# Kernel tuning notes

Hardware: AMD Instinct MI355X
Metric: run time of the kernel (lower is better)

## Reference

```python
import jax, jax.numpy as jnp
import numpy as np

BN_EPS = 1e-5
NN_EPS = 1e-8

def _bn_relu(h, gamma, beta):
    # training-mode BatchNorm1d over (B, L) per channel, biased variance
    mean = jnp.mean(h, axis=(0, 2), keepdims=True)
    var = jnp.mean((h - mean) ** 2, axis=(0, 2), keepdims=True)
    hn = (h - mean) * jax.lax.rsqrt(var + BN_EPS)
    return jax.nn.relu(hn * gamma[None, :, None] + beta[None, :, None])

def setup_inputs() -> dict:
    key = jax.random.key(0)
    ks = jax.random.split(key, 8)
    B, N, M, Cin, Cout = 2, 2048, 8192, 512, 256
    return {
        "x1": jax.random.normal(ks[0], (B, N, Cin), jnp.float32),
        "p1": jax.random.uniform(ks[1], (B, N, 3), jnp.float32),
        "x2": jax.random.normal(ks[2], (B, M, Cout), jnp.float32),
        "p2": jax.random.uniform(ks[3], (B, M, 3), jnp.float32),
        "W_up": jax.random.normal(ks[4], (Cout, Cin), jnp.float32) * (1.0 / np.sqrt(Cin)),
        "gamma_up": jnp.ones((Cout,), jnp.float32),
        "beta_up": jnp.zeros((Cout,), jnp.float32),
        "W_lat": jax.random.normal(ks[5], (Cout, Cout), jnp.float32) * (1.0 / np.sqrt(Cout)),
        "gamma_lat": jnp.ones((Cout,), jnp.float32),
        "beta_lat": jnp.zeros((Cout,), jnp.float32),
    }

def reference(x1, p1, x2, p2, W_up, gamma_up, beta_up, W_lat, gamma_lat, beta_lat):
    B, M, _ = p2.shape
    # up_mlp: 1x1 conv (bias=False) + BN + ReLU -> (B, Cout, N)
    h1 = _bn_relu(jnp.einsum('bnc,oc->bon', x1, W_up), gamma_up, beta_up)
    # three_nn: squared distances from each p2 query to all p1 points
    d2 = (jnp.sum(p2 ** 2, -1)[:, :, None] + jnp.sum(p1 ** 2, -1)[:, None, :]
          - 2.0 * jnp.einsum('bmd,bnd->bmn', p2, p1))  # (B, M, N)
    neg_d, idx = jax.lax.top_k(-d2, 3)                 # 3 smallest squared dists
    dist = -neg_d                                      # (B, M, 3)
    dist_recip = 1.0 / (dist + NN_EPS)
    weight = dist_recip / jnp.sum(dist_recip, axis=2, keepdims=True)  # (B, M, 3)
    # three_interpolate: weighted gather of h1 along point axis
    C = h1.shape[1]
    g = jnp.take_along_axis(h1, idx.reshape(B, 1, M * 3), axis=2).reshape(B, C, M, 3)
    interp = jnp.einsum('bcmk,bmk->bcm', g, weight)    # (B, Cout, M)
    # lateral_mlp on x2
    h2 = _bn_relu(jnp.einsum('bmc,oc->bom', x2, W_lat), gamma_lat, beta_lat)
    y = interp + h2                                    # (B, Cout, M)
    return jnp.transpose(y, (0, 2, 1)), p2             # (B, M, Cout), (B, M, 3)
```

## Files before the change

kernel.cpp:

```cpp
#include <hip/hip_runtime.h>

#define BATCH 2
#define NPTS  2048
#define MPTS  8192
#define CIN1  512
#define CIN2  256
#define COUT  256
#define ROWS1 (BATCH*NPTS)
#define ROWS2 (BATCH*MPTS)
#define BN_EPS 1e-5f
#define NN_EPS 1e-8f

#define NCHUNK 16
#define CHUNK  (NPTS / NCHUNK)

typedef __attribute__((ext_vector_type(8))) short  bf16x8;
typedef __attribute__((ext_vector_type(4))) float  f32x4;

__device__ __forceinline__ unsigned short bf16_rne(float x) {
    unsigned u = __float_as_uint(x);
    u += 0x7FFFu + ((u >> 16) & 1u);
    return (unsigned short)(u >> 16);
}
__device__ __forceinline__ float bf16_f32(unsigned short h) {
    return __uint_as_float(((unsigned)h) << 16);
}
__device__ __forceinline__ void split2(float x, unsigned short& h, unsigned short& l) {
    h = bf16_rne(x);
    l = bf16_rne(x - bf16_f32(h));
}

template<int K, int KSPLIT, bool FUSE_STATS>
__global__ __launch_bounds__(256)
void gemm_mfma64(const float* __restrict__ A, const float* __restrict__ W,
                 float* __restrict__ C, float* __restrict__ stats) {
    constexpr int BK = 32;
    constexpr int LDK = 40;
    constexpr int KCH = K / KSPLIT;
    __shared__ unsigned short Ah[64][LDK], Al[64][LDK];
    __shared__ unsigned short Bh[64][LDK], Bl[64][LDK];
    __shared__ float red[64][8];

    const int tid = threadIdx.x;
    const int m0 = blockIdx.y * 64;
    const int o0 = blockIdx.x * 64;
    const int kbase = blockIdx.z * KCH;
    const int lane = tid & 63, wid = tid >> 6;
    const int wy = wid >> 1, wx = wid & 1;
    const int lr = lane & 15, lg = lane >> 4;
    const int srow = tid >> 3;
    const int squad = (tid & 7) * 4;

    f32x4 acc[2][2];
    #pragma unroll
    for (int i = 0; i < 2; ++i)
        #pragma unroll
        for (int j = 0; j < 2; ++j)
            acc[i][j] = (f32x4){0.f, 0.f, 0.f, 0.f};

    const float* Abase = A + (size_t)m0 * K + kbase + squad;
    const float* Wbase = W + (size_t)o0 * K + kbase + squad;

    for (int k0 = 0; k0 < KCH; k0 += BK) {
        __syncthreads();
        #pragma unroll
        for (int rr = 0; rr < 2; ++rr) {
            const int r = srow + rr * 32;
            float4 va = *(const float4*)(Abase + (size_t)r * K + k0);
            float4 vb = *(const float4*)(Wbase + (size_t)r * K + k0);
            ushort4 h, l;
            split2(va.x, h.x, l.x); split2(va.y, h.y, l.y);
            split2(va.z, h.z, l.z); split2(va.w, h.w, l.w);
            *(ushort4*)&Ah[r][squad] = h;
            *(ushort4*)&Al[r][squad] = l;
            split2(vb.x, h.x, l.x); split2(vb.y, h.y, l.y);
            split2(vb.z, h.z, l.z); split2(vb.w, h.w, l.w);
            *(ushort4*)&Bh[r][squad] = h;
            *(ushort4*)&Bl[r][squad] = l;
        }
        __syncthreads();

        bf16x8 fah[2], fal[2], fbh[2], fbl[2];
        #pragma unroll
        for (int i = 0; i < 2; ++i) {
            const int row = wy * 32 + i * 16 + lr;
            fah[i] = *(const bf16x8*)&Ah[row][lg * 8];
            fal[i] = *(const bf16x8*)&Al[row][lg * 8];
        }
        #pragma unroll
        for (int j = 0; j < 2; ++j) {
            const int row = wx * 32 + j * 16 + lr;
            fbh[j] = *(const bf16x8*)&Bh[row][lg * 8];
            fbl[j] = *(const bf16x8*)&Bl[row][lg * 8];
        }
        #pragma unroll
        for (int i = 0; i < 2; ++i)
            #pragma unroll
            for (int j = 0; j < 2; ++j) {
                acc[i][j] = __builtin_amdgcn_mfma_f32_16x16x32_bf16(fah[i], fbh[j], acc[i][j], 0, 0, 0);
                acc[i][j] = __builtin_amdgcn_mfma_f32_16x16x32_bf16(fal[i], fbh[j], acc[i][j], 0, 0, 0);
                acc[i][j] = __builtin_amdgcn_mfma_f32_16x16x32_bf16(fah[i], fbl[j], acc[i][j], 0, 0, 0);
            }
    }

    #pragma unroll
    for (int i = 0; i < 2; ++i)
        #pragma unroll
        for (int j = 0; j < 2; ++j) {
            const int col = o0 + wx * 32 + j * 16 + lr;
            const int rbase = m0 + wy * 32 + i * 16 + lg * 4;
            #pragma unroll
            for (int r = 0; r < 4; ++r) {
                if (KSPLIT > 1)
                    atomicAdd(&C[(size_t)(rbase + r) * COUT + col], acc[i][j][r]);
                else
                    C[(size_t)(rbase + r) * COUT + col] = acc[i][j][r];
            }
        }

    if constexpr (FUSE_STATS) {
        #pragma unroll
        for (int j = 0; j < 2; ++j) {
            float s = 0.f;
            #pragma unroll
            for (int i = 0; i < 2; ++i)
                #pragma unroll
                for (int r = 0; r < 4; ++r)
                    s += acc[i][j][r];
            red[wx * 32 + j * 16 + lr][wy * 4 + lg] = s;
        }
        __syncthreads();
        if (tid < 64) {
            float s = 0.f;
            #pragma unroll
            for (int k = 0; k < 8; ++k) s += red[tid][k];
            atomicAdd(&stats[o0 + tid], s);
        }
        __syncthreads();
        #pragma unroll
        for (int j = 0; j < 2; ++j) {
            float q = 0.f;
            #pragma unroll
            for (int i = 0; i < 2; ++i)
                #pragma unroll
                for (int r = 0; r < 4; ++r)
                    q = fmaf(acc[i][j][r], acc[i][j][r], q);
            red[wx * 32 + j * 16 + lr][wy * 4 + lg] = q;
        }
        __syncthreads();
        if (tid < 64) {
            float q = 0.f;
            #pragma unroll
            for (int k = 0; k < 8; ++k) q += red[tid][k];
            atomicAdd(&stats[COUT + o0 + tid], q);
        }
    }
}

__global__ __launch_bounds__(256)
void colsum256(const float* __restrict__ X, int rowsPerBlock,
               float* __restrict__ out) {
    const int c = threadIdx.x;
    const int r0 = blockIdx.x * rowsPerBlock;
    float s = 0.f, q = 0.f;
    for (int r = 0; r < rowsPerBlock; ++r) {
        float v = X[(size_t)(r0 + r) * COUT + c];
        s += v;
        q = fmaf(v, v, q);
    }
    atomicAdd(&out[c], s);
    atomicAdd(&out[COUT + c], q);
}

__global__ __launch_bounds__(256)
void three_nn_part(const float* __restrict__ p1, const float* __restrict__ p2,
                   float2* __restrict__ part) {
    __shared__ float4 pts[CHUNK];
    const int b = blockIdx.z;
    const int c = blockIdx.y;
    const int t = threadIdx.x;
    const int n0 = c * CHUNK;
    if (t < CHUNK) {
        const float* P1 = p1 + ((size_t)b * NPTS + n0) * 3;
        float x = P1[t * 3 + 0], y = P1[t * 3 + 1], z = P1[t * 3 + 2];
        pts[t] = make_float4(x, y, z, x * x + y * y + z * z);
    }
    __syncthreads();
    const int m = blockIdx.x * 256 + t;
    const float* q = p2 + ((size_t)b * MPTS + m) * 3;
    const float qx = q[0], qy = q[1], qz = q[2];
    const float s2 = qx * qx + qy * qy + qz * qz;
    float d0 = 1e30f, d1 = 1e30f, d2 = 1e30f;
    int   i0 = 0,     i1 = 0,     i2 = 0;
    #pragma unroll 4
    for (int n = 0; n < CHUNK; ++n) {
        float4 p = pts[n];
        float dot = p.x * qx + p.y * qy + p.z * qz;
        float d = s2 + p.w - 2.0f * dot;
        if (d < d2) {
            if (d < d1) {
                d2 = d1; i2 = i1;
                if (d < d0) { d1 = d0; i1 = i0; d0 = d; i0 = n0 + n; }
                else        { d1 = d;  i1 = n0 + n; }
            } else { d2 = d; i2 = n0 + n; }
        }
    }
    float2* o = part + ((size_t)(b * MPTS + m) * NCHUNK + c) * 3;
    o[0] = make_float2(d0, __int_as_float(i0));
    o[1] = make_float2(d1, __int_as_float(i1));
    o[2] = make_float2(d2, __int_as_float(i2));
}

__global__ __launch_bounds__(256)
void three_nn_merge(const float2* __restrict__ part,
                    int* __restrict__ idx, float* __restrict__ wgt) {
    const int row = blockIdx.x * 256 + threadIdx.x;
    const float4* pp = (const float4*)(part + (size_t)row * NCHUNK * 3);
    float d0 = 1e30f, d1 = 1e30f, d2 = 1e30f;
    int   i0 = 0,     i1 = 0,     i2 = 0;
    #pragma unroll
    for (int j = 0; j < NCHUNK * 3 / 2; ++j) {
        float4 v = pp[j];
        #pragma unroll
        for (int h = 0; h < 2; ++h) {
            float d = h ? v.z : v.x;
            int   i = __float_as_int(h ? v.w : v.y);
            if (d < d2) {
                if (d < d1) {
                    d2 = d1; i2 = i1;
                    if (d < d0) { d1 = d0; i1 = i0; d0 = d; i0 = i; }
                    else        { d1 = d;  i1 = i; }
                } else { d2 = d; i2 = i; }
            }
        }
    }
    const float r0 = 1.0f / (d0 + NN_EPS);
    const float r1 = 1.0f / (d1 + NN_EPS);
    const float r2 = 1.0f / (d2 + NN_EPS);
    const float rs = r0 + r1 + r2;
    const size_t o = (size_t)row * 3;
    idx[o + 0] = i0; idx[o + 1] = i1; idx[o + 2] = i2;
    wgt[o + 0] = r0 / rs; wgt[o + 1] = r1 / rs; wgt[o + 2] = r2 / rs;
}

__global__ __launch_bounds__(256)
void final_combine(const float* __restrict__ h1, const float* __restrict__ stats,
                   const float* __restrict__ g1, const float* __restrict__ b1,
                   const float* __restrict__ g2, const float* __restrict__ b2,
                   const int* __restrict__ idx, const float* __restrict__ wgt,
                   float* __restrict__ out) {
    const int t = threadIdx.x;
    const int row = blockIdx.x * 4 + (t >> 6);
    const int c = (t & 63) * 4;
    const int b = row >> 13;

    const float4 sum1 = *(const float4*)&stats[c];
    const float4 sq1  = *(const float4*)&stats[COUT + c];
    const float4 sum2 = *(const float4*)&stats[512 + c];
    const float4 sq2  = *(const float4*)&stats[768 + c];
    const float4 gg1  = *(const float4*)&g1[c];
    const float4 bb1  = *(const float4*)&b1[c];
    const float4 gg2  = *(const float4*)&g2[c];
    const float4 bb2  = *(const float4*)&b2[c];

    const float inv1 = 1.0f / (float)ROWS1, inv2 = 1.0f / (float)ROWS2;
    float4 sc1, sh1, sc2, sh2;
    {
        float m, v;
        m = sum1.x*inv1; v = fmaf(-m,m,sq1.x*inv1); sc1.x = gg1.x/sqrtf(v+BN_EPS); sh1.x = fmaf(-m,sc1.x,bb1.x);
        m = sum1.y*inv1; v = fmaf(-m,m,sq1.y*inv1); sc1.y = gg1.y/sqrtf(v+BN_EPS); sh1.y = fmaf(-m,sc1.y,bb1.y);
        m = sum1.z*inv1; v = fmaf(-m,m,sq1.z*inv1); sc1.z = gg1.z/sqrtf(v+BN_EPS); sh1.z = fmaf(-m,sc1.z,bb1.z);
        m = sum1.w*inv1; v = fmaf(-m,m,sq1.w*inv1); sc1.w = gg1.w/sqrtf(v+BN_EPS); sh1.w = fmaf(-m,sc1.w,bb1.w);
        m = sum2.x*inv2; v = fmaf(-m,m,sq2.x*inv2); sc2.x = gg2.x/sqrtf(v+BN_EPS); sh2.x = fmaf(-m,sc2.x,bb2.x);
        m = sum2.y*inv2; v = fmaf(-m,m,sq2.y*inv2); sc2.y = gg2.y/sqrtf(v+BN_EPS); sh2.y = fmaf(-m,sc2.y,bb2.y);
        m = sum2.z*inv2; v = fmaf(-m,m,sq2.z*inv2); sc2.z = gg2.z/sqrtf(v+BN_EPS); sh2.z = fmaf(-m,sc2.z,bb2.z);
        m = sum2.w*inv2; v = fmaf(-m,m,sq2.w*inv2); sc2.w = gg2.w/sqrtf(v+BN_EPS); sh2.w = fmaf(-m,sc2.w,bb2.w);
    }

    const size_t o3 = (size_t)row * 3;
    const int i0 = idx[o3 + 0], i1 = idx[o3 + 1], i2 = idx[o3 + 2];
    const float w0 = wgt[o3 + 0], w1 = wgt[o3 + 1], w2 = wgt[o3 + 2];
    const float* hb = h1 + (size_t)b * NPTS * COUT + c;
    const float4 h0 = *(const float4*)(hb + (size_t)i0 * COUT);
    const float4 h4 = *(const float4*)(hb + (size_t)i1 * COUT);
    const float4 h8 = *(const float4*)(hb + (size_t)i2 * COUT);

    const size_t oi = (size_t)row * COUT + c;
    float4 yv = *(const float4*)&out[oi];
    float4 r;
    r.x = fmaxf(fmaf(yv.x, sc2.x, sh2.x), 0.f)
        + w0 * fmaxf(fmaf(h0.x, sc1.x, sh1.x), 0.f)
        + w1 * fmaxf(fmaf(h4.x, sc1.x, sh1.x), 0.f)
        + w2 * fmaxf(fmaf(h8.x, sc1.x, sh1.x), 0.f);
    r.y = fmaxf(fmaf(yv.y, sc2.y, sh2.y), 0.f)
        + w0 * fmaxf(fmaf(h0.y, sc1.y, sh1.y), 0.f)
        + w1 * fmaxf(fmaf(h4.y, sc1.y, sh1.y), 0.f)
        + w2 * fmaxf(fmaf(h8.y, sc1.y, sh1.y), 0.f);
    r.z = fmaxf(fmaf(yv.z, sc2.z, sh2.z), 0.f)
        + w0 * fmaxf(fmaf(h0.z, sc1.z, sh1.z), 0.f)
        + w1 * fmaxf(fmaf(h4.z, sc1.z, sh1.z), 0.f)
        + w2 * fmaxf(fmaf(h8.z, sc1.z, sh1.z), 0.f);
    r.w = fmaxf(fmaf(yv.w, sc2.w, sh2.w), 0.f)
        + w0 * fmaxf(fmaf(h0.w, sc1.w, sh1.w), 0.f)
        + w1 * fmaxf(fmaf(h4.w, sc1.w, sh1.w), 0.f)
        + w2 * fmaxf(fmaf(h8.w, sc1.w, sh1.w), 0.f);
    *(float4*)&out[oi] = r;
}

extern "C" void kernel_launch(void* const* d_in, const int* in_sizes, int n_in,
                              void* d_out, int out_size, void* d_ws, size_t ws_size,
                              hipStream_t stream) {
    const float* x1       = (const float*)d_in[0];
    const float* p1       = (const float*)d_in[1];
    const float* x2       = (const float*)d_in[2];
    const float* p2       = (const float*)d_in[3];
    const float* W_up     = (const float*)d_in[4];
    const float* gamma_up = (const float*)d_in[5];
    const float* beta_up  = (const float*)d_in[6];
    const float* W_lat    = (const float*)d_in[7];
    const float* gamma_lat= (const float*)d_in[8];
    const float* beta_lat = (const float*)d_in[9];
    float* out = (float*)d_out;

    float*  h1    = (float*)d_ws;
    float*  stats = h1 + (size_t)ROWS1 * COUT;
    int*    idx   = (int*)(stats + 1024);
    float*  wgt   = (float*)(idx + (size_t)ROWS2 * 3);
    float2* part  = (float2*)(wgt + (size_t)ROWS2 * 3);

    hipMemsetAsync(stats, 0, 1024 * sizeof(float), stream);
    hipMemsetAsync(h1, 0, (size_t)ROWS1 * COUT * sizeof(float), stream);

    gemm_mfma64<CIN1, 4, false><<<dim3(COUT / 64, ROWS1 / 64, 4), 256, 0, stream>>>(
        x1, W_up, h1, nullptr);
    colsum256<<<256, 256, 0, stream>>>(h1, ROWS1 / 256, stats);

    gemm_mfma64<CIN2, 1, true><<<dim3(COUT / 64, ROWS2 / 64, 1), 256, 0, stream>>>(
        x2, W_lat, out, stats + 512);

    three_nn_part<<<dim3(MPTS / 256, NCHUNK, BATCH), 256, 0, stream>>>(p1, p2, part);
    three_nn_merge<<<ROWS2 / 256, 256, 0, stream>>>(part, idx, wgt);

    final_combine<<<ROWS2 / 4, 256, 0, stream>>>(h1, stats, gamma_up, beta_up,
                                                 gamma_lat, beta_lat, idx, wgt, out);

    hipMemcpyAsync(out + (size_t)ROWS2 * COUT, p2,
                   (size_t)ROWS2 * 3 * sizeof(float),
                   hipMemcpyDeviceToDevice, stream);
}
```

Baseline: 179.7 us.

## Prefetch GEMM tiles, stage epilogue via LDS, fuse three_nn merge into combine

The GEMM now loads the next K-tile from global memory into registers while the current tile is consumed by MFMA, and writes its results through a shared-memory tile so the stores (or split-K atomics) are coalesced float4 rows, with BN statistics computed from that tile in a single reduction pass. The separate three_nn_merge kernel is removed and its top-3 merge plus weight computation is folded into final_combine, which removes one launch and the idx/wgt round trip. The trade-off is that every one of the 64 threads serving a row repeats the 48-entry merge over the partial results, and the epilogue needs extra LDS traffic and barriers.

New measurement: 234.4 us. 30.4% more time.

```diff
diff --git a/kernel.cpp b/kernel.cpp
--- a/kernel.cpp
+++ b/kernel.cpp
@@ -37,9 +37,10 @@
     constexpr int BK = 32;
     constexpr int LDK = 40;
     constexpr int KCH = K / KSPLIT;
-    __shared__ unsigned short Ah[64][LDK], Al[64][LDK];
-    __shared__ unsigned short Bh[64][LDK], Bl[64][LDK];
-    __shared__ float red[64][8];
+    __shared__ union {
+        struct { unsigned short Ah[64][LDK], Al[64][LDK], Bh[64][LDK], Bl[64][LDK]; } s;
+        struct { float Ct[64][68]; float red[64][8]; } e;
+    } U;
 
     const int tid = threadIdx.x;
     const int m0 = blockIdx.y * 64;
@@ -48,7 +49,7 @@
     const int lane = tid & 63, wid = tid >> 6;
     const int wy = wid >> 1, wx = wid & 1;
     const int lr = lane & 15, lg = lane >> 4;
-    const int srow = tid >> 3;
+    const int sr = tid >> 3;
     const int squad = (tid & 7) * 4;
 
     f32x4 acc[2][2];
@@ -61,37 +62,53 @@
     const float* Abase = A + (size_t)m0 * K + kbase + squad;
     const float* Wbase = W + (size_t)o0 * K + kbase + squad;
 
+    float4 va0 = *(const float4*)(Abase + (size_t)sr * K);
+    float4 va1 = *(const float4*)(Abase + (size_t)(sr + 32) * K);
+    float4 vb0 = *(const float4*)(Wbase + (size_t)sr * K);
+    float4 vb1 = *(const float4*)(Wbase + (size_t)(sr + 32) * K);
+
     for (int k0 = 0; k0 < KCH; k0 += BK) {
         __syncthreads();
-        #pragma unroll
-        for (int rr = 0; rr < 2; ++rr) {
-            const int r = srow + rr * 32;
-            float4 va = *(const float4*)(Abase + (size_t)r * K + k0);
-            float4 vb = *(const float4*)(Wbase + (size_t)r * K + k0);
+        {
             ushort4 h, l;
-            split2(va.x, h.x, l.x); split2(va.y, h.y, l.y);
-            split2(va.z, h.z, l.z); split2(va.w, h.w, l.w);
-            *(ushort4*)&Ah[r][squad] = h;
-            *(ushort4*)&Al[r][squad] = l;
-            split2(vb.x, h.x, l.x); split2(vb.y, h.y, l.y);
-            split2(vb.z, h.z, l.z); split2(vb.w, h.w, l.w);
-            *(ushort4*)&Bh[r][squad] = h;
-            *(ushort4*)&Bl[r][squad] = l;
+            split2(va0.x, h.x, l.x); split2(va0.y, h.y, l.y);
+            split2(va0.z, h.z, l.z); split2(va0.w, h.w, l.w);
+            *(ushort4*)&U.s.Ah[sr][squad] = h;
+            *(ushort4*)&U.s.Al[sr][squad] = l;
+            split2(va1.x, h.x, l.x); split2(va1.y, h.y, l.y);
+            split2(va1.z, h.z, l.z); split2(va1.w, h.w, l.w);
+            *(ushort4*)&U.s.Ah[sr + 32][squad] = h;
+            *(ushort4*)&U.s.Al[sr + 32][squad] = l;
+            split2(vb0.x, h.x, l.x); split2(vb0.y, h.y, l.y);
+            split2(vb0.z, h.z, l.z); split2(vb0.w, h.w, l.w);
+            *(ushort4*)&U.s.Bh[sr][squad] = h;
+            *(ushort4*)&U.s.Bl[sr][squad] = l;
+            split2(vb1.x, h.x, l.x); split2(vb1.y, h.y, l.y);
+            split2(vb1.z, h.z, l.z); split2(vb1.w, h.w, l.w);
+            *(ushort4*)&U.s.Bh[sr + 32][squad] = h;
+            *(ushort4*)&U.s.Bl[sr + 32][squad] = l;
         }
         __syncthreads();
+
+        if (k0 + BK < KCH) {
+            va0 = *(const float4*)(Abase + (size_t)sr * K + k0 + BK);
+            va1 = *(const float4*)(Abase + (size_t)(sr + 32) * K + k0 + BK);
+            vb0 = *(const float4*)(Wbase + (size_t)sr * K + k0 + BK);
+            vb1 = *(const float4*)(Wbase + (size_t)(sr + 32) * K + k0 + BK);
+        }
 
         bf16x8 fah[2], fal[2], fbh[2], fbl[2];
         #pragma unroll
         for (int i = 0; i < 2; ++i) {
             const int row = wy * 32 + i * 16 + lr;
-            fah[i] = *(const bf16x8*)&Ah[row][lg * 8];
-            fal[i] = *(const bf16x8*)&Al[row][lg * 8];
+            fah[i] = *(const bf16x8*)&U.s.Ah[row][lg * 8];
+            fal[i] = *(const bf16x8*)&U.s.Al[row][lg * 8];
         }
         #pragma unroll
         for (int j = 0; j < 2; ++j) {
             const int row = wx * 32 + j * 16 + lr;
-            fbh[j] = *(const bf16x8*)&Bh[row][lg * 8];
-            fbl[j] = *(const bf16x8*)&Bl[row][lg * 8];
+            fbh[j] = *(const bf16x8*)&U.s.Bh[row][lg * 8];
+            fbl[j] = *(const bf16x8*)&U.s.Bl[row][lg * 8];
         }
         #pragma unroll
         for (int i = 0; i < 2; ++i)
@@ -103,56 +120,53 @@
             }
     }
 
+    __syncthreads();
     #pragma unroll
     for (int i = 0; i < 2; ++i)
         #pragma unroll
         for (int j = 0; j < 2; ++j) {
-            const int col = o0 + wx * 32 + j * 16 + lr;
-            const int rbase = m0 + wy * 32 + i * 16 + lg * 4;
+            const int col = wx * 32 + j * 16 + lr;
+            const int rbase = wy * 32 + i * 16 + lg * 4;
             #pragma unroll
-            for (int r = 0; r < 4; ++r) {
-                if (KSPLIT > 1)
-                    atomicAdd(&C[(size_t)(rbase + r) * COUT + col], acc[i][j][r]);
-                else
-                    C[(size_t)(rbase + r) * COUT + col] = acc[i][j][r];
+            for (int r = 0; r < 4; ++r)
+                U.e.Ct[rbase + r][col] = acc[i][j][r];
+        }
+    __syncthreads();
+
+    {
+        const int cr = tid >> 4;
+        const int cc = (tid & 15) * 4;
+        #pragma unroll
+        for (int q = 0; q < 4; ++q) {
+            const int row = cr + q * 16;
+            float4 v = *(const float4*)&U.e.Ct[row][cc];
+            float* dst = &C[(size_t)(m0 + row) * COUT + o0 + cc];
+            if (KSPLIT > 1) {
+                atomicAdd(dst + 0, v.x); atomicAdd(dst + 1, v.y);
+                atomicAdd(dst + 2, v.z); atomicAdd(dst + 3, v.w);
+            } else {
+                *(float4*)dst = v;
             }
         }
+    }
 
     if constexpr (FUSE_STATS) {
-        #pragma unroll
-        for (int j = 0; j < 2; ++j) {
-            float s = 0.f;
-            #pragma unroll
-            for (int i = 0; i < 2; ++i)
-                #pragma unroll
-                for (int r = 0; r < 4; ++r)
-                    s += acc[i][j][r];
-            red[wx * 32 + j * 16 + lr][wy * 4 + lg] = s;
-        }
+        const int col = tid & 63, rq = tid >> 6;
+        float s = 0.f, q2 = 0.f;
+        #pragma unroll
+        for (int r = 0; r < 16; ++r) {
+            float v = U.e.Ct[rq * 16 + r][col];
+            s += v;
+            q2 = fmaf(v, v, q2);
+        }
+        U.e.red[col][rq] = s;
+        U.e.red[col][4 + rq] = q2;
         __syncthreads();
         if (tid < 64) {
-            float s = 0.f;
-            #pragma unroll
-            for (int k = 0; k < 8; ++k) s += red[tid][k];
-            atomicAdd(&stats[o0 + tid], s);
-        }
-        __syncthreads();
-        #pragma unroll
-        for (int j = 0; j < 2; ++j) {
-            float q = 0.f;
-            #pragma unroll
-            for (int i = 0; i < 2; ++i)
-                #pragma unroll
-                for (int r = 0; r < 4; ++r)
-                    q = fmaf(acc[i][j][r], acc[i][j][r], q);
-            red[wx * 32 + j * 16 + lr][wy * 4 + lg] = q;
-        }
-        __syncthreads();
-        if (tid < 64) {
-            float q = 0.f;
-            #pragma unroll
-            for (int k = 0; k < 8; ++k) q += red[tid][k];
-            atomicAdd(&stats[COUT + o0 + tid], q);
+            float ss = U.e.red[tid][0] + U.e.red[tid][1] + U.e.red[tid][2] + U.e.red[tid][3];
+            float qq = U.e.red[tid][4] + U.e.red[tid][5] + U.e.red[tid][6] + U.e.red[tid][7];
+            atomicAdd(&stats[o0 + tid], ss);
+            atomicAdd(&stats[COUT + o0 + tid], qq);
         }
     }
 }
@@ -212,47 +226,41 @@
 }
 
 __global__ __launch_bounds__(256)
-void three_nn_merge(const float2* __restrict__ part,
-                    int* __restrict__ idx, float* __restrict__ wgt) {
-    const int row = blockIdx.x * 256 + threadIdx.x;
-    const float4* pp = (const float4*)(part + (size_t)row * NCHUNK * 3);
-    float d0 = 1e30f, d1 = 1e30f, d2 = 1e30f;
-    int   i0 = 0,     i1 = 0,     i2 = 0;
-    #pragma unroll
-    for (int j = 0; j < NCHUNK * 3 / 2; ++j) {
-        float4 v = pp[j];
-        #pragma unroll
-        for (int h = 0; h < 2; ++h) {
-            float d = h ? v.z : v.x;
-            int   i = __float_as_int(h ? v.w : v.y);
-            if (d < d2) {
-                if (d < d1) {
-                    d2 = d1; i2 = i1;
-                    if (d < d0) { d1 = d0; i1 = i0; d0 = d; i0 = i; }
-                    else        { d1 = d;  i1 = i; }
-                } else { d2 = d; i2 = i; }
-            }
-        }
-    }
-    const float r0 = 1.0f / (d0 + NN_EPS);
-    const float r1 = 1.0f / (d1 + NN_EPS);
-    const float r2 = 1.0f / (d2 + NN_EPS);
-    const float rs = r0 + r1 + r2;
-    const size_t o = (size_t)row * 3;
-    idx[o + 0] = i0; idx[o + 1] = i1; idx[o + 2] = i2;
-    wgt[o + 0] = r0 / rs; wgt[o + 1] = r1 / rs; wgt[o + 2] = r2 / rs;
-}
-
-__global__ __launch_bounds__(256)
 void final_combine(const float* __restrict__ h1, const float* __restrict__ stats,
                    const float* __restrict__ g1, const float* __restrict__ b1,
                    const float* __restrict__ g2, const float* __restrict__ b2,
-                   const int* __restrict__ idx, const float* __restrict__ wgt,
-                   float* __restrict__ out) {
+                   const float2* __restrict__ part, float* __restrict__ out) {
     const int t = threadIdx.x;
     const int row = blockIdx.x * 4 + (t >> 6);
     const int c = (t & 63) * 4;
     const int b = row >> 13;
+
+    float d0 = 1e30f, d1 = 1e30f, d2 = 1e30f;
+    int   i0 = 0,     i1 = 0,     i2 = 0;
+    {
+        const float4* pp = (const float4*)(part + (size_t)row * NCHUNK * 3);
+        #pragma unroll
+        for (int j = 0; j < NCHUNK * 3 / 2; ++j) {
+            float4 v = pp[j];
+            #pragma unroll
+            for (int h = 0; h < 2; ++h) {
+                float d = h ? v.z : v.x;
+                int   i = __float_as_int(h ? v.w : v.y);
+                if (d < d2) {
+                    if (d < d1) {
+                        d2 = d1; i2 = i1;
+                        if (d < d0) { d1 = d0; i1 = i0; d0 = d; i0 = i; }
+                        else        { d1 = d;  i1 = i; }
+                    } else { d2 = d; i2 = i; }
+                }
+            }
+        }
+    }
+    const float r0 = 1.0f / (d0 + NN_EPS);
+    const float r1 = 1.0f / (d1 + NN_EPS);
+    const float r2 = 1.0f / (d2 + NN_EPS);
+    const float irs = 1.0f / (r0 + r1 + r2);
+    const float w0 = r0 * irs, w1 = r1 * irs, w2 = r2 * irs;
 
     const float4 sum1 = *(const float4*)&stats[c];
     const float4 sq1  = *(const float4*)&stats[COUT + c];
@@ -277,9 +285,6 @@
         m = sum2.w*inv2; v = fmaf(-m,m,sq2.w*inv2); sc2.w = gg2.w/sqrtf(v+BN_EPS); sh2.w = fmaf(-m,sc2.w,bb2.w);
     }
 
-    const size_t o3 = (size_t)row * 3;
-    const int i0 = idx[o3 + 0], i1 = idx[o3 + 1], i2 = idx[o3 + 2];
-    const float w0 = wgt[o3 + 0], w1 = wgt[o3 + 1], w2 = wgt[o3 + 2];
     const float* hb = h1 + (size_t)b * NPTS * COUT + c;
     const float4 h0 = *(const float4*)(hb + (size_t)i0 * COUT);
     const float4 h4 = *(const float4*)(hb + (size_t)i1 * COUT);
@@ -324,9 +329,7 @@
 
     float*  h1    = (float*)d_ws;
     float*  stats = h1 + (size_t)ROWS1 * COUT;
-    int*    idx   = (int*)(stats + 1024);
-    float*  wgt   = (float*)(idx + (size_t)ROWS2 * 3);
-    float2* part  = (float2*)(wgt + (size_t)ROWS2 * 3);
+    float2* part  = (float2*)(stats + 1024);
 
     hipMemsetAsync(stats, 0, 1024 * sizeof(float), stream);
     hipMemsetAsync(h1, 0, (size_t)ROWS1 * COUT * sizeof(float), stream);
@@ -339,10 +342,9 @@
         x2, W_lat, out, stats + 512);
 
     three_nn_part<<<dim3(MPTS / 256, NCHUNK, BATCH), 256, 0, stream>>>(p1, p2, part);
-    three_nn_merge<<<ROWS2 / 256, 256, 0, stream>>>(part, idx, wgt);
 
     final_combine<<<ROWS2 / 4, 256, 0, stream>>>(h1, stats, gamma_up, beta_up,
-                                                 gamma_lat, beta_lat, idx, wgt, out);
+                                                 gamma_lat, beta_lat, part, out);
 
     hipMemcpyAsync(out + (size_t)ROWS2 * COUT, p2,
                    (size_t)ROWS2 * 3 * sizeof(float),
```

## Pre-split GEMM inputs to bf16 tiles, stream via global_load_lds, fuse NN merge

Applied to the files above, without the earlier changes.

A new pre-pass kernel splits the activations and weights once into swizzled bf16 hi/lo tile images in workspace. The GEMMs then double-buffer these tiles straight into LDS with global_load_lds, so the split arithmetic leaves the inner loop and the loads overlap the MFMAs. The three-NN merge moves into final_combine, which removes one launch and the idx/wgt round trip. The costs are an extra pass that writes 2x bf16 copies of every input, and each of the 64 threads per row in the combine now redoes the 48-entry merge on its own.

New measurement: 194.7 us. +8.3%, slower.

```diff
diff --git a/kernel.cpp b/kernel.cpp
--- a/kernel.cpp
+++ b/kernel.cpp
@@ -17,6 +17,9 @@
 typedef __attribute__((ext_vector_type(8))) short  bf16x8;
 typedef __attribute__((ext_vector_type(4))) float  f32x4;
 
+#define AS1 __attribute__((address_space(1)))
+#define AS3 __attribute__((address_space(3)))
+
 __device__ __forceinline__ unsigned short bf16_rne(float x) {
     unsigned u = __float_as_uint(x);
     u += 0x7FFFu + ((u >> 16) & 1u);
@@ -25,31 +28,69 @@
 __device__ __forceinline__ float bf16_f32(unsigned short h) {
     return __uint_as_float(((unsigned)h) << 16);
 }
-__device__ __forceinline__ void split2(float x, unsigned short& h, unsigned short& l) {
-    h = bf16_rne(x);
-    l = bf16_rne(x - bf16_f32(h));
-}
-
-template<int K, int KSPLIT, bool FUSE_STATS>
+
+__device__ __forceinline__ void gload16(const void* g, void* l) {
+    __builtin_amdgcn_global_load_lds((const AS1 unsigned int*)g,
+                                     (AS3 unsigned int*)l, 16, 0, 0);
+}
+
 __global__ __launch_bounds__(256)
-void gemm_mfma64(const float* __restrict__ A, const float* __restrict__ W,
-                 float* __restrict__ C, float* __restrict__ stats) {
-    constexpr int BK = 32;
-    constexpr int LDK = 40;
-    constexpr int KCH = K / KSPLIT;
-    __shared__ unsigned short Ah[64][LDK], Al[64][LDK];
-    __shared__ unsigned short Bh[64][LDK], Bl[64][LDK];
+void split_pre(const float* __restrict__ x1, const float* __restrict__ x2,
+               const float* __restrict__ wu, const float* __restrict__ wl,
+               unsigned short* __restrict__ x1h, unsigned short* __restrict__ x1l,
+               unsigned short* __restrict__ x2h, unsigned short* __restrict__ x2l,
+               unsigned short* __restrict__ wuh, unsigned short* __restrict__ wul,
+               unsigned short* __restrict__ wlh, unsigned short* __restrict__ wll) {
+    const int bid = blockIdx.x;
+    const float* src; unsigned short *dh, *dl; int K, tile;
+    if (bid < 1024)      { src = x1; dh = x1h; dl = x1l; K = CIN1; tile = bid; }
+    else if (bid < 3072) { src = x2; dh = x2h; dl = x2l; K = CIN2; tile = bid - 1024; }
+    else if (bid < 3136) { src = wu; dh = wuh; dl = wul; K = CIN1; tile = bid - 3072; }
+    else                 { src = wl; dh = wlh; dl = wll; K = CIN2; tile = bid - 3136; }
+    const int ktiles = K / 32;
+    const int rt = tile / ktiles, kt = tile - rt * ktiles;
+    const int t = threadIdx.x, row = t >> 2, lg = t & 3;
+
+    const float* s = src + (size_t)(rt * 64 + row) * K + kt * 32 + lg * 8;
+    const float4 v0 = *(const float4*)s;
+    const float4 v1 = *(const float4*)(s + 4);
+    const float vv[8] = {v0.x, v0.y, v0.z, v0.w, v1.x, v1.y, v1.z, v1.w};
+    bf16x8 h, l;
+    #pragma unroll
+    for (int i = 0; i < 8; ++i) {
+        const unsigned short hh = bf16_rne(vv[i]);
+        h[i] = (short)hh;
+        l[i] = (short)bf16_rne(vv[i] - bf16_f32(hh));
+    }
+    const unsigned off = ((unsigned)(row * 64 + lg * 16)) ^ ((unsigned)((row & 7) << 4));
+    *(bf16x8*)((char*)dh + (size_t)tile * 4096 + off) = h;
+    *(bf16x8*)((char*)dl + (size_t)tile * 4096 + off) = l;
+}
+
+template<int KTILES, int KSPLIT, bool FUSE_STATS>
+__global__ __launch_bounds__(256)
+void gemm_pre(const unsigned short* __restrict__ Ah_img, const unsigned short* __restrict__ Al_img,
+              const unsigned short* __restrict__ Bh_img, const unsigned short* __restrict__ Bl_img,
+              float* __restrict__ C, float* __restrict__ stats) {
+    constexpr int KT = KTILES / KSPLIT;
+    __shared__ __align__(16) unsigned char lds[2][4][4096];
     __shared__ float red[64][8];
 
     const int tid = threadIdx.x;
-    const int m0 = blockIdx.y * 64;
-    const int o0 = blockIdx.x * 64;
-    const int kbase = blockIdx.z * KCH;
     const int lane = tid & 63, wid = tid >> 6;
+    const int m0 = blockIdx.y * 64, o0 = blockIdx.x * 64;
+    const int kt0 = blockIdx.z * KT;
     const int wy = wid >> 1, wx = wid & 1;
     const int lr = lane & 15, lg = lane >> 4;
-    const int srow = tid >> 3;
-    const int squad = (tid & 7) * 4;
+
+    const unsigned short* src;
+    size_t base;
+    switch (wid) {
+        case 0:  src = Ah_img; base = ((size_t)blockIdx.y * KTILES + kt0) * 2048; break;
+        case 1:  src = Al_img; base = ((size_t)blockIdx.y * KTILES + kt0) * 2048; break;
+        case 2:  src = Bh_img; base = ((size_t)blockIdx.x * KTILES + kt0) * 2048; break;
+        default: src = Bl_img; base = ((size_t)blockIdx.x * KTILES + kt0) * 2048; break;
+    }
 
     f32x4 acc[2][2];
     #pragma unroll
@@ -58,40 +99,44 @@
         for (int j = 0; j < 2; ++j)
             acc[i][j] = (f32x4){0.f, 0.f, 0.f, 0.f};
 
-    const float* Abase = A + (size_t)m0 * K + kbase + squad;
-    const float* Wbase = W + (size_t)o0 * K + kbase + squad;
-
-    for (int k0 = 0; k0 < KCH; k0 += BK) {
-        __syncthreads();
-        #pragma unroll
-        for (int rr = 0; rr < 2; ++rr) {
-            const int r = srow + rr * 32;
-            float4 va = *(const float4*)(Abase + (size_t)r * K + k0);
-            float4 vb = *(const float4*)(Wbase + (size_t)r * K + k0);
-            ushort4 h, l;
-            split2(va.x, h.x, l.x); split2(va.y, h.y, l.y);
-            split2(va.z, h.z, l.z); split2(va.w, h.w, l.w);
-            *(ushort4*)&Ah[r][squad] = h;
-            *(ushort4*)&Al[r][squad] = l;
-            split2(vb.x, h.x, l.x); split2(vb.y, h.y, l.y);
-            split2(vb.z, h.z, l.z); split2(vb.w, h.w, l.w);
-            *(ushort4*)&Bh[r][squad] = h;
-            *(ushort4*)&Bl[r][squad] = l;
-        }
-        __syncthreads();
+    auto STAGE = [&](int buf, int t) {
+        const unsigned short* s = src + base + (size_t)t * 2048;
+        char* l = (char*)&lds[buf][wid][0];
+        #pragma unroll
+        for (int c = 0; c < 4; ++c)
+            gload16(s + c * 512 + lane * 8, l + c * 1024);
+    };
+
+    auto FOFF = [&](int row) -> int {
+        return (row * 64 + lg * 16) ^ ((row & 7) << 4);
+    };
+
+    STAGE(0, 0);
+    asm volatile("s_waitcnt vmcnt(0)" ::: "memory");
+    __builtin_amdgcn_s_barrier();
+    __builtin_amdgcn_sched_barrier(0);
+
+    int cur = 0;
+    for (int t = 0; t < KT; ++t) {
+        if (t + 1 < KT) STAGE(cur ^ 1, t + 1);
+
+        const char* LAh = (const char*)&lds[cur][0][0];
+        const char* LAl = (const char*)&lds[cur][1][0];
+        const char* LBh = (const char*)&lds[cur][2][0];
+        const char* LBl = (const char*)&lds[cur][3][0];
 
         bf16x8 fah[2], fal[2], fbh[2], fbl[2];
         #pragma unroll
         for (int i = 0; i < 2; ++i) {
-            const int row = wy * 32 + i * 16 + lr;
-            fah[i] = *(const bf16x8*)&Ah[row][lg * 8];
-            fal[i] = *(const bf16x8*)&Al[row][lg * 8];
+            const int off = FOFF(wy * 32 + i * 16 + lr);
+            fah[i] = *(const bf16x8*)(LAh + off);
+            fal[i] = *(const bf16x8*)(LAl + off);
         }
         #pragma unroll
         for (int j = 0; j < 2; ++j) {
-            const int row = wx * 32 + j * 16 + lr;
-            fbh[j] = *(const bf16x8*)&Bh[row][lg * 8];
-            fbl[j] = *(const bf16x8*)&Bl[row][lg * 8];
+            const int off = FOFF(wx * 32 + j * 16 + lr);
+            fbh[j] = *(const bf16x8*)(LBh + off);
+            fbl[j] = *(const bf16x8*)(LBl + off);
         }
         #pragma unroll
         for (int i = 0; i < 2; ++i)
@@ -101,6 +146,11 @@
                 acc[i][j] = __builtin_amdgcn_mfma_f32_16x16x32_bf16(fal[i], fbh[j], acc[i][j], 0, 0, 0);
                 acc[i][j] = __builtin_amdgcn_mfma_f32_16x16x32_bf16(fah[i], fbl[j], acc[i][j], 0, 0, 0);
             }
+
+        asm volatile("s_waitcnt vmcnt(0)" ::: "memory");
+        __builtin_amdgcn_s_barrier();
+        __builtin_amdgcn_sched_barrier(0);
+        cur ^= 1;
     }
 
     #pragma unroll
@@ -212,47 +262,41 @@
 }
 
 __global__ __launch_bounds__(256)
-void three_nn_merge(const float2* __restrict__ part,
-                    int* __restrict__ idx, float* __restrict__ wgt) {
-    const int row = blockIdx.x * 256 + threadIdx.x;
-    const float4* pp = (const float4*)(part + (size_t)row * NCHUNK * 3);
-    float d0 = 1e30f, d1 = 1e30f, d2 = 1e30f;
-    int   i0 = 0,     i1 = 0,     i2 = 0;
-    #pragma unroll
-    for (int j = 0; j < NCHUNK * 3 / 2; ++j) {
-        float4 v = pp[j];
-        #pragma unroll
-        for (int h = 0; h < 2; ++h) {
-            float d = h ? v.z : v.x;
-            int   i = __float_as_int(h ? v.w : v.y);
-            if (d < d2) {
-                if (d < d1) {
-                    d2 = d1; i2 = i1;
-                    if (d < d0) { d1 = d0; i1 = i0; d0 = d; i0 = i; }
-                    else        { d1 = d;  i1 = i; }
-                } else { d2 = d; i2 = i; }
-            }
-        }
-    }
-    const float r0 = 1.0f / (d0 + NN_EPS);
-    const float r1 = 1.0f / (d1 + NN_EPS);
-    const float r2 = 1.0f / (d2 + NN_EPS);
-    const float rs = r0 + r1 + r2;
-    const size_t o = (size_t)row * 3;
-    idx[o + 0] = i0; idx[o + 1] = i1; idx[o + 2] = i2;
-    wgt[o + 0] = r0 / rs; wgt[o + 1] = r1 / rs; wgt[o + 2] = r2 / rs;
-}
-
-__global__ __launch_bounds__(256)
 void final_combine(const float* __restrict__ h1, const float* __restrict__ stats,
                    const float* __restrict__ g1, const float* __restrict__ b1,
                    const float* __restrict__ g2, const float* __restrict__ b2,
-                   const int* __restrict__ idx, const float* __restrict__ wgt,
-                   float* __restrict__ out) {
+                   const float2* __restrict__ part, float* __restrict__ out) {
     const int t = threadIdx.x;
     const int row = blockIdx.x * 4 + (t >> 6);
     const int c = (t & 63) * 4;
     const int b = row >> 13;
+
+    float d0 = 1e30f, d1 = 1e30f, d2 = 1e30f;
+    int   i0 = 0,     i1 = 0,     i2 = 0;
+    {
+        const float4* pp = (const float4*)(part + (size_t)row * NCHUNK * 3);
+        #pragma unroll
+        for (int j = 0; j < NCHUNK * 3 / 2; ++j) {
+            float4 v = pp[j];
+            #pragma unroll
+            for (int h = 0; h < 2; ++h) {
+                float d = h ? v.z : v.x;
+                int   i = __float_as_int(h ? v.w : v.y);
+                if (d < d2) {
+                    if (d < d1) {
+                        d2 = d1; i2 = i1;
+                        if (d < d0) { d1 = d0; i1 = i0; d0 = d; i0 = i; }
+                        else        { d1 = d;  i1 = i; }
+                    } else { d2 = d; i2 = i; }
+                }
+            }
+        }
+    }
+    const float r0 = 1.0f / (d0 + NN_EPS);
+    const float r1 = 1.0f / (d1 + NN_EPS);
+    const float r2 = 1.0f / (d2 + NN_EPS);
+    const float irs = 1.0f / (r0 + r1 + r2);
+    const float w0 = r0 * irs, w1 = r1 * irs, w2 = r2 * irs;
 
     const float4 sum1 = *(const float4*)&stats[c];
     const float4 sq1  = *(const float4*)&stats[COUT + c];
@@ -277,9 +321,6 @@
         m = sum2.w*inv2; v = fmaf(-m,m,sq2.w*inv2); sc2.w = gg2.w/sqrtf(v+BN_EPS); sh2.w = fmaf(-m,sc2.w,bb2.w);
     }
 
-    const size_t o3 = (size_t)row * 3;
-    const int i0 = idx[o3 + 0], i1 = idx[o3 + 1], i2 = idx[o3 + 2];
-    const float w0 = wgt[o3 + 0], w1 = wgt[o3 + 1], w2 = wgt[o3 + 2];
     const float* hb = h1 + (size_t)b * NPTS * COUT + c;
     const float4 h0 = *(const float4*)(hb + (size_t)i0 * COUT);
     const float4 h4 = *(const float4*)(hb + (size_t)i1 * COUT);
@@ -322,27 +363,36 @@
     const float* beta_lat = (const float*)d_in[9];
     float* out = (float*)d_out;
 
-    float*  h1    = (float*)d_ws;
-    float*  stats = h1 + (size_t)ROWS1 * COUT;
-    int*    idx   = (int*)(stats + 1024);
-    float*  wgt   = (float*)(idx + (size_t)ROWS2 * 3);
-    float2* part  = (float2*)(wgt + (size_t)ROWS2 * 3);
+    char* w = (char*)d_ws;
+    unsigned short* x1h = (unsigned short*)(w);
+    unsigned short* x1l = (unsigned short*)(w + (4u<<20));
+    unsigned short* x2h = (unsigned short*)(w + (8u<<20));
+    unsigned short* x2l = (unsigned short*)(w + (16u<<20));
+    unsigned short* wuh = (unsigned short*)(w + (24u<<20));
+    unsigned short* wul = (unsigned short*)(w + (24u<<20) + (256u<<10));
+    unsigned short* wlh = (unsigned short*)(w + (24u<<20) + (512u<<10));
+    unsigned short* wll = (unsigned short*)(w + (24u<<20) + (640u<<10));
+    float*  h1    = (float*)(w + (25u<<20));
+    float*  stats = (float*)(w + (29u<<20));
+    float2* part  = (float2*)(w + (29u<<20) + (16u<<10));
 
     hipMemsetAsync(stats, 0, 1024 * sizeof(float), stream);
     hipMemsetAsync(h1, 0, (size_t)ROWS1 * COUT * sizeof(float), stream);
 
-    gemm_mfma64<CIN1, 4, false><<<dim3(COUT / 64, ROWS1 / 64, 4), 256, 0, stream>>>(
-        x1, W_up, h1, nullptr);
+    split_pre<<<3168, 256, 0, stream>>>(x1, x2, W_up, W_lat,
+                                        x1h, x1l, x2h, x2l, wuh, wul, wlh, wll);
+
+    gemm_pre<CIN1/32, 4, false><<<dim3(COUT/64, ROWS1/64, 4), 256, 0, stream>>>(
+        x1h, x1l, wuh, wul, h1, nullptr);
     colsum256<<<256, 256, 0, stream>>>(h1, ROWS1 / 256, stats);
 
-    gemm_mfma64<CIN2, 1, true><<<dim3(COUT / 64, ROWS2 / 64, 1), 256, 0, stream>>>(
-        x2, W_lat, out, stats + 512);
+    gemm_pre<CIN2/32, 1, true><<<dim3(COUT/64, ROWS2/64, 1), 256, 0, stream>>>(
+        x2h, x2l, wlh, wll, out, stats + 512);
 
     three_nn_part<<<dim3(MPTS / 256, NCHUNK, BATCH), 256, 0, stream>>>(p1, p2, part);
-    three_nn_merge<<<ROWS2 / 256, 256, 0, stream>>>(part, idx, wgt);
 
     final_combine<<<ROWS2 / 4, 256, 0, stream>>>(h1, stats, gamma_up, beta_up,
-                                                 gamma_lat, beta_lat, idx, wgt, out);
+                                                 gamma_lat, beta_lat, part, out);
 
     hipMemcpyAsync(out + (size_t)ROWS2 * COUT, p2,
                    (size_t)ROWS2 * 3 * sizeof(float),
```
